# Kernel optimization log

Hardware: AMD Instinct MI355X
Metric: run time of the kernel (lower is better)

## Reference

```python
import jax, jax.numpy as jnp
import numpy as np
import math

B, L, D = 2, 2048, 1024
H, HD = 16, 64          # num heads, head dim
R = 256                 # kv lora rank = D // 4
E, K, F = 8, 2, 1024    # routed experts, top_k, intermediate size


def rmsnorm(x, w, eps=1e-6):
    ms = jnp.mean(x * x, axis=-1, keepdims=True)
    return w * (x * jax.lax.rsqrt(ms + eps))


def setup_inputs() -> dict:
    key = jax.random.key(0)
    ks = jax.random.split(key, 16)
    s = 0.02
    return {
        "x": jax.random.normal(ks[0], (B, L, D), jnp.float32),
        "ln1_w": jnp.ones((D,), jnp.float32),
        "q_w": jax.random.normal(ks[1], (D, H * HD), jnp.float32) * s,
        "kvd_w": jax.random.normal(ks[2], (D, R), jnp.float32) * s,
        "kvn_w": jnp.ones((R,), jnp.float32),
        "kvu_w": jax.random.normal(ks[3], (R, 2 * H * HD), jnp.float32) * s,
        "o_w": jax.random.normal(ks[4], (H * HD, D), jnp.float32) * s,
        "ln2_w": jnp.ones((D,), jnp.float32),
        "gate_w": jax.random.normal(ks[5], (D, E), jnp.float32) * s,
        "sh_w1": jax.random.normal(ks[6], (D, F), jnp.float32) * s,
        "sh_w2": jax.random.normal(ks[7], (F, D), jnp.float32) * s,
        "sh_w3": jax.random.normal(ks[8], (D, F), jnp.float32) * s,
        "re_w1": jax.random.normal(ks[9], (E, D, F), jnp.float32) * s,
        "re_w2": jax.random.normal(ks[10], (E, F, D), jnp.float32) * s,
        "re_w3": jax.random.normal(ks[11], (E, D, F), jnp.float32) * s,
    }


def reference(x, ln1_w, q_w, kvd_w, kvn_w, kvu_w, o_w, ln2_w, gate_w,
              sh_w1, sh_w2, sh_w3, re_w1, re_w2, re_w3):
    # ---- MLHA attention with pre-RMSNorm and latent-compressed KV ----
    xn = rmsnorm(x, ln1_w)
    q = (xn @ q_w).reshape(B, L, H, HD)
    latent = rmsnorm(xn @ kvd_w, kvn_w)                 # [B,L,R]
    kv = latent @ kvu_w                                 # [B,L,2*H*HD]
    k, v = jnp.split(kv, 2, axis=-1)
    k = k.reshape(B, L, H, HD)
    v = v.reshape(B, L, H, HD)
    scores = jnp.einsum('bxhd,byhd->bhxy', q, k) / math.sqrt(HD)
    causal = jnp.tril(jnp.ones((L, L), bool))
    scores = jnp.where(causal, scores, -jnp.inf)
    attn = jax.nn.softmax(scores, axis=-1)
    attn_out = jnp.einsum('bhxy,byhd->bxhd', attn, v).reshape(B, L, H * HD)
    h = x + attn_out @ o_w

    # ---- MoE (inference: no jitter, expert_bias = 0, no bias update) ----
    hn = rmsnorm(h, ln2_w)
    flat = hn.reshape(-1, D)                            # [T,D], T=B*L
    # shared expert (SwiGLU)
    shared = (jax.nn.silu(flat @ sh_w1) * (flat @ sh_w3)) @ sh_w2
    # router
    logits = flat @ gate_w                              # [T,E]
    probs = jax.nn.softmax(logits, axis=-1)
    topw, topi = jax.lax.top_k(probs, K)                # [T,K]
    topw = topw / jnp.sum(topw, axis=-1, keepdims=True)
    # per-token per-expert combine weight [T,E]
    combine = jnp.sum(topw[..., None] * jax.nn.one_hot(topi, E, dtype=flat.dtype), axis=1)
    # all routed experts densely, then masked combine (same math as masked loop)
    h1 = jnp.einsum('td,edf->etf', flat, re_w1)
    h3 = jnp.einsum('td,edf->etf', flat, re_w3)
    eo = jnp.einsum('etf,efd->etd', jax.nn.silu(h1) * h3, re_w2)
    routed = jnp.einsum('te,etd->td', combine, eo)
    moe_out = (shared + routed).reshape(B, L, D)
    return h + moe_out, probs
```

## Files before the change

### kernel.cpp

```cpp
#include <hip/hip_runtime.h>
#include <hip/hip_bf16.h>
#include <cstdint>
#include <cstddef>

typedef unsigned short u16;
typedef unsigned int u32;
typedef __attribute__((ext_vector_type(8))) short bf16x8;
typedef __attribute__((ext_vector_type(4))) float f32x4;

static constexpr int Bb = 2, Ll = 2048, Dd = 1024, Hh = 16, Rr = 256, Ee = 8, Ff = 1024;
static constexpr int Tt = Bb * Ll;
static constexpr float QSCALE = 0.18033688011112042f;

__device__ __forceinline__ u16 f2bf(float f){
  union { float f; u32 u; } v; v.f = f;
  u32 u = v.u;
  u32 r = u + 0x7FFFu + ((u >> 16) & 1u);
  return (u16)(r >> 16);
}
__device__ __forceinline__ float bf2f(u16 b){
  union { u32 u; float f; } v; v.u = ((u32)b) << 16; return v.f;
}

#define GLDS(gp, lp) __builtin_amdgcn_global_load_lds( \
    (const __attribute__((address_space(1))) unsigned int*)(gp), \
    (__attribute__((address_space(3))) unsigned int*)(lp), 16, 0, 0)

__global__ void transpose5(const float* __restrict__ q_w, const float* __restrict__ o_w,
                           const float* __restrict__ w1, const float* __restrict__ w3,
                           const float* __restrict__ w2,
                           u16* __restrict__ qkvdT, u16* __restrict__ oT,
                           u16* __restrict__ sh13T, u16* __restrict__ sh2T){
  const float* s; u16* d; int off, str;
  switch (blockIdx.z){
    case 0: s = q_w; d = qkvdT; off = 0; str = 1; break;
    case 1: s = o_w; d = oT;    off = 0; str = 1; break;
    case 2: s = w1;  d = sh13T; off = 0; str = 2; break;
    case 3: s = w3;  d = sh13T; off = 1; str = 2; break;
    default: s = w2; d = sh2T;  off = 0; str = 1; break;
  }
  __shared__ float tile[32][33];
  int bx = blockIdx.x * 32, by = blockIdx.y * 32;
  int tx = threadIdx.x, ty = threadIdx.y;
  #pragma unroll
  for (int i = ty; i < 32; i += 8) tile[i][tx] = s[(size_t)(by + i) * 1024 + bx + tx];
  __syncthreads();
  #pragma unroll
  for (int i = ty; i < 32; i += 8)
    d[(size_t)(off + (bx + i) * str) * 1024 + by + tx] = f2bf(tile[tx][i]);
}

__global__ void transposeEx(const float* __restrict__ re_w1, const float* __restrict__ re_w3,
                            const float* __restrict__ re_w2,
                            u16* __restrict__ re13T, u16* __restrict__ re2T){
  int z = blockIdx.z, which = z >> 3, e = z & 7;
  const float* s; u16* d; int off, str;
  size_t eo = (size_t)e * 1024 * 1024;
  if (which == 0){ s = re_w1 + eo; d = re13T + (size_t)e * 2048 * 1024; off = 0; str = 2; }
  else if (which == 1){ s = re_w3 + eo; d = re13T + (size_t)e * 2048 * 1024; off = 1; str = 2; }
  else { s = re_w2 + eo; d = re2T + (size_t)e * 1024 * 1024; off = 0; str = 1; }
  __shared__ float tile[32][33];
  int bx = blockIdx.x * 32, by = blockIdx.y * 32;
  int tx = threadIdx.x, ty = threadIdx.y;
  #pragma unroll
  for (int i = ty; i < 32; i += 8) tile[i][tx] = s[(size_t)(by + i) * 1024 + bx + tx];
  __syncthreads();
  #pragma unroll
  for (int i = ty; i < 32; i += 8)
    d[(size_t)(off + (bx + i) * str) * 1024 + by + tx] = f2bf(tile[tx][i]);
}

__global__ void transpose_conv(const float* __restrict__ src, u16* __restrict__ dst,
                               int K, int N, int dstOff){
  __shared__ float tile[32][33];
  int bx = blockIdx.x * 32, by = blockIdx.y * 32;
  int tx = threadIdx.x, ty = threadIdx.y;
  #pragma unroll
  for (int i = ty; i < 32; i += 8) tile[i][tx] = src[(size_t)(by + i) * N + bx + tx];
  __syncthreads();
  #pragma unroll
  for (int i = ty; i < 32; i += 8)
    dst[(size_t)(dstOff + bx + i) * K + by + tx] = f2bf(tile[tx][i]);
}

template<int DIM>
__global__ void rmsnorm_kernel(const float* __restrict__ x, const float* __restrict__ w,
                               u16* __restrict__ out){
  int t = blockIdx.x;
  const float* xr = x + (size_t)t * DIM;
  u16* orow = out + (size_t)t * DIM;
  int tid = threadIdx.x;
  constexpr int NT = 256;
  constexpr int PER = DIM / NT > 0 ? DIM / NT : 1;
  float vals[PER];
  float ss = 0.f;
  #pragma unroll
  for (int i = 0; i < PER; i++){
    int d = tid + i * NT;
    float v = (d < DIM) ? xr[d] : 0.f;
    vals[i] = v; ss += v * v;
  }
  __shared__ float red[4];
  for (int m = 32; m; m >>= 1) ss += __shfl_xor(ss, m, 64);
  if ((tid & 63) == 0) red[tid >> 6] = ss;
  __syncthreads();
  float tot = red[0] + red[1] + red[2] + red[3];
  float rn = rsqrtf(tot / DIM + 1e-6f);
  #pragma unroll
  for (int i = 0; i < PER; i++){
    int d = tid + i * NT;
    if (d < DIM) orow[d] = f2bf(vals[i] * rn * w[d]);
  }
}

__global__ void router_kernel(const float* __restrict__ h, const float* __restrict__ ln2w,
                              const float* __restrict__ gate,
                              float* __restrict__ probs_out,
                              int* __restrict__ topi, float* __restrict__ topw,
                              u16* __restrict__ hn){
  int t = blockIdx.x; int tid = threadIdx.x;
  const float* hr = h + (size_t)t * Dd;
  float v[4]; float ss = 0.f;
  #pragma unroll
  for (int i = 0; i < 4; i++){ float x = hr[tid + i * 256]; v[i] = x; ss += x * x; }
  __shared__ float red[4];
  for (int m = 32; m; m >>= 1) ss += __shfl_xor(ss, m, 64);
  if ((tid & 63) == 0) red[tid >> 6] = ss;
  __syncthreads();
  float rn = rsqrtf((red[0] + red[1] + red[2] + red[3]) / Dd + 1e-6f);
  float p[8];
  #pragma unroll
  for (int e = 0; e < 8; e++) p[e] = 0.f;
  #pragma unroll
  for (int i = 0; i < 4; i++){
    int d = tid + i * 256;
    float hv = v[i] * rn * ln2w[d];
    hn[(size_t)t * Dd + d] = f2bf(hv);
    const float* g = gate + (size_t)d * 8;
    #pragma unroll
    for (int e = 0; e < 8; e++) p[e] += hv * g[e];
  }
  #pragma unroll
  for (int e = 0; e < 8; e++){
    float x = p[e];
    for (int m = 32; m; m >>= 1) x += __shfl_xor(x, m, 64);
    p[e] = x;
  }
  __shared__ float pe[4][8];
  if ((tid & 63) == 0){ for (int e = 0; e < 8; e++) pe[tid >> 6][e] = p[e]; }
  __syncthreads();
  if (tid == 0){
    float lg[8];
    for (int e = 0; e < 8; e++) lg[e] = pe[0][e] + pe[1][e] + pe[2][e] + pe[3][e];
    float mx = lg[0];
    for (int e = 1; e < 8; e++) mx = fmaxf(mx, lg[e]);
    float pr[8]; float s = 0.f;
    for (int e = 0; e < 8; e++){ pr[e] = __expf(lg[e] - mx); s += pr[e]; }
    float inv = 1.f / s;
    for (int e = 0; e < 8; e++) probs_out[(size_t)t * 8 + e] = pr[e] * inv;
    int i0 = 0;
    for (int e = 1; e < 8; e++) if (pr[e] > pr[i0]) i0 = e;
    int i1 = -1;
    for (int e = 0; e < 8; e++){ if (e == i0) continue; if (i1 < 0 || pr[e] > pr[i1]) i1 = e; }
    float w0 = pr[i0], w1 = pr[i1]; float wn = 1.f / (w0 + w1);
    topi[t * 2] = i0; topi[t * 2 + 1] = i1;
    topw[t * 2] = w0 * wn; topw[t * 2 + 1] = w1 * wn;
  }
}

__global__ void hist_kernel(const int* __restrict__ topi, int* __restrict__ counts){
  __shared__ int h[8];
  int tid = threadIdx.x;
  if (tid < 8) h[tid] = 0;
  __syncthreads();
  int base = blockIdx.x * 512;
  for (int i = tid; i < 512; i += 256) atomicAdd(&h[topi[base + i]], 1);
  __syncthreads();
  if (tid < 8) atomicAdd(&counts[tid], h[tid]);
}

__global__ void bucket_kernel(const int* __restrict__ topi, const float* __restrict__ topw,
                              const int* __restrict__ counts, int* __restrict__ cur,
                              int* __restrict__ entries, float* __restrict__ ew){
  __shared__ int lh[8], lbase[8], lcur[8], loffs[8];
  int tid = threadIdx.x;
  if (tid < 8) lh[tid] = 0;
  __syncthreads();
  int t = blockIdx.x * 256 + tid;
  int e0 = topi[t * 2], e1 = topi[t * 2 + 1];
  atomicAdd(&lh[e0], 1); atomicAdd(&lh[e1], 1);
  __syncthreads();
  if (tid == 0){
    int c = 0;
    for (int e = 0; e < 8; e++){ loffs[e] = c; c += counts[e]; }
  }
  if (tid < 8){ lbase[tid] = atomicAdd(&cur[tid], lh[tid]); lcur[tid] = 0; }
  __syncthreads();
  int p0 = atomicAdd(&lcur[e0], 1);
  int pos0 = loffs[e0] + lbase[e0] + p0;
  entries[pos0] = t; ew[pos0] = topw[t * 2];
  int p1 = atomicAdd(&lcur[e1], 1);
  int pos1 = loffs[e1] + lbase[e1] + p1;
  entries[pos1] = t; ew[pos1] = topw[t * 2 + 1];
}

template<int TM, int ROWMODE, int MODE>
__launch_bounds__(256)
__global__ void gemm_bt(const u16* __restrict__ A, const u16* __restrict__ Bt,
                        void* __restrict__ C, const float* __restrict__ res,
                        int M, int N, int K, int lda, int ldc,
                        const int* __restrict__ entries, const float* __restrict__ ew,
                        const int* __restrict__ counts,
                        float* __restrict__ outAt){
  constexpr int MTC = TM / 32;
  __shared__ __align__(16) u16 As[TM * 32];
  __shared__ __align__(16) u16 Bs[128 * 32];
  __shared__ int els[TM];
  __shared__ float ewl[TM];

  int e = (ROWMODE ? blockIdx.z : 0);
  const u16* Bte = Bt + (size_t)e * N * K;
  int cnt, off;
  if (ROWMODE == 0){ cnt = M; off = 0; }
  else {
    cnt = counts[e];
    off = 0;
    for (int i = 0; i < e; i++) off += counts[i];
  }
  int rt = blockIdx.y * TM;
  if (rt >= cnt) return;
  int cb = blockIdx.x * 128;
  int tid = threadIdx.x;

  if (ROWMODE >= 1){
    if (tid < TM){
      int r = rt + tid;
      els[tid] = (r < cnt) ? entries[off + r] : 0;
      ewl[tid] = (MODE == 4 && r < cnt) ? ew[off + r] : 0.f;
    }
    __syncthreads();
  }

  int sr = tid >> 2;
  int skc = (tid & 3) * 8;
  int rr0 = rt + sr, rr1 = rt + sr + 64;
  size_t ar0 = 0, ar1 = 0;
  if (ROWMODE == 0){ ar0 = (size_t)rr0; ar1 = (size_t)rr1; }
  else if (ROWMODE == 1){ ar0 = (size_t)els[sr];
                          ar1 = (TM == 128) ? (size_t)els[sr + 64] : 0; }
  else {
    int c0 = rr0 < cnt ? rr0 : (cnt - 1);
    int c1 = rr1 < cnt ? rr1 : (cnt - 1);
    ar0 = (size_t)off + c0; ar1 = (size_t)off + c1;
  }
  const u16* pa0 = A + ar0 * lda + skc;
  const u16* pa1 = A + ar1 * lda + skc;
  const u16* pb0 = Bte + (size_t)(cb + sr) * K + skc;
  const u16* pb1 = Bte + (size_t)(cb + sr + 64) * K + skc;
  u16* lA0 = &As[tid * 8];
  u16* lA1 = &As[(TM == 128 ? 2048 : 0) + tid * 8];
  u16* lB0 = &Bs[tid * 8];
  u16* lB1 = &Bs[2048 + tid * 8];

  int w = tid >> 6, lane = tid & 63;
  int wm = w >> 1, wn = w & 1;
  int quad = lane >> 4, l16 = lane & 15;

  f32x4 acc[MTC][4];
  const f32x4 zf = {0.f, 0.f, 0.f, 0.f};
  #pragma unroll
  for (int i = 0; i < MTC; i++)
    #pragma unroll
    for (int j = 0; j < 4; j++) acc[i][j] = zf;

  for (int k0 = 0; k0 < K; k0 += 32){
    __syncthreads();
    GLDS(pa0 + k0, lA0);
    if (TM == 128) GLDS(pa1 + k0, lA1);
    GLDS(pb0 + k0, lB0);
    GLDS(pb1 + k0, lB1);
    __syncthreads();
    bf16x8 af[MTC], bfr[4];
    #pragma unroll
    for (int mt = 0; mt < MTC; mt++)
      af[mt] = *(const bf16x8*)&As[(wm * (TM / 2) + mt * 16 + l16) * 32 + quad * 8];
    #pragma unroll
    for (int nt = 0; nt < 4; nt++)
      bfr[nt] = *(const bf16x8*)&Bs[(wn * 64 + nt * 16 + l16) * 32 + quad * 8];
    #pragma unroll
    for (int mt = 0; mt < MTC; mt++)
      #pragma unroll
      for (int nt = 0; nt < 4; nt++)
        acc[mt][nt] = __builtin_amdgcn_mfma_f32_16x16x32_bf16(af[mt], bfr[nt], acc[mt][nt], 0, 0, 0);
  }

  #pragma unroll
  for (int mt = 0; mt < MTC; mt++){
    #pragma unroll
    for (int nt = 0; nt < 4; nt++){
      #pragma unroll
      for (int r = 0; r < 4; r++){
        int row = wm * (TM / 2) + mt * 16 + quad * 4 + r;
        int col = cb + wn * 64 + nt * 16 + l16;
        int rr = rt + row;
        float v = acc[mt][nt][r];
        if (MODE == 6){
          float pv = __shfl_xor(v, 1, 64);
          if (rr < cnt && (l16 & 1) == 0){
            float sl = v / (1.f + __expf(-v));
            size_t crow = (size_t)((ROWMODE == 1) ? (off + rr) : rr);
            ((u16*)C)[crow * ldc + (col >> 1)] = f2bf(sl * pv);
          }
          continue;
        }
        if (rr >= cnt) continue;
        if (MODE == 0){
          size_t ci = (size_t)((ROWMODE == 1) ? (off + rr) : rr) * ldc + col;
          ((u16*)C)[ci] = f2bf(v);
        } else if (MODE == 1){
          size_t ci = (size_t)rr * ldc + col;
          ((float*)C)[ci] = v + res[ci];
        } else if (MODE == 5){
          if (col < 1024) ((u16*)C)[(size_t)rr * 1024 + col] = f2bf(v * QSCALE);
          else            outAt[(size_t)rr * 256 + (col - 1024)] = v;
        } else {
          int tok = els[row];
          atomicAdd(&outAt[(size_t)tok * ldc + col], ewl[row] * v);
        }
      }
    }
  }
}

#define RBAR() __builtin_amdgcn_s_barrier()
#define VMCNT8() do{ asm volatile("s_waitcnt vmcnt(8)" ::: "memory"); \
                     __builtin_amdgcn_sched_barrier(0); }while(0)
#define VMCNT0() do{ asm volatile("s_waitcnt vmcnt(0)" ::: "memory"); \
                     __builtin_amdgcn_sched_barrier(0); }while(0)
#define MMQ(MQ, NQ, FA, FB) do{ \
  _Pragma("unroll") \
  for (int m4_ = 0; m4_ < 4; m4_++){ \
    _Pragma("unroll") \
    for (int n2_ = 0; n2_ < 2; n2_++){ \
      acc[(MQ)*4+m4_][(NQ)*2+n2_] = __builtin_amdgcn_mfma_f32_16x16x32_bf16(FA[m4_][0], FB[n2_][0], acc[(MQ)*4+m4_][(NQ)*2+n2_], 0, 0, 0); \
      acc[(MQ)*4+m4_][(NQ)*2+n2_] = __builtin_amdgcn_mfma_f32_16x16x32_bf16(FA[m4_][1], FB[n2_][1], acc[(MQ)*4+m4_][(NQ)*2+n2_], 0, 0, 0); \
    } \
  } }while(0)
#define RDA(DST, BB, MQ) do{ \
  _Pragma("unroll") \
  for (int m4_ = 0; m4_ < 4; m4_++){ \
    const char* p_ = (const char*)(&As[BB][0]) + (size_t)(wm*128 + (MQ)*64 + m4_*16 + l16)*128; \
    DST[m4_][0] = *(const bf16x8*)(p_ + offk0); \
    DST[m4_][1] = *(const bf16x8*)(p_ + offk1); \
  } }while(0)
#define RDB(DST, BB, NQ) do{ \
  _Pragma("unroll") \
  for (int n2_ = 0; n2_ < 2; n2_++){ \
    const char* p_ = (const char*)(&Bs[BB][0]) + (size_t)(wn*64 + (NQ)*32 + n2_*16 + l16)*128; \
    DST[n2_][0] = *(const bf16x8*)(p_ + offk0); \
    DST[n2_][1] = *(const bf16x8*)(p_ + offk1); \
  } }while(0)
#define STGA(SB, H, KT) do{ \
  GLDS(gA[(H)*2+0] + (size_t)(KT)*64, &As[SB][((H)*128 +  0)*64] + (size_t)tid*8); \
  GLDS(gA[(H)*2+1] + (size_t)(KT)*64, &As[SB][((H)*128 + 64)*64] + (size_t)tid*8); }while(0)
#define STGB(SB, H, KT) do{ \
  GLDS(gB[(H)*2+0] + (size_t)(KT)*64, &Bs[SB][((H)*128 +  0)*64] + (size_t)tid*8); \
  GLDS(gB[(H)*2+1] + (size_t)(KT)*64, &Bs[SB][((H)*128 + 64)*64] + (size_t)tid*8); }while(0)

__launch_bounds__(512, 2)
__global__ void gemm256_up(const u16* __restrict__ A,
                           const u16* __restrict__ sh13, const u16* __restrict__ re13,
                           u16* __restrict__ shg, u16* __restrict__ gr,
                           const int* __restrict__ entries, const int* __restrict__ counts){
  __shared__ __align__(16) u16 As[2][256 * 64];
  __shared__ __align__(16) u16 Bs[2][256 * 64];

  int e = blockIdx.z;
  int cnt, off = 0;
  if (e < 8){
    cnt = counts[e];
    for (int i = 0; i < e; i++) off += counts[i];
  } else cnt = Tt;
  int rt = blockIdx.y * 256;
  if (rt >= cnt) return;
  int cb = blockIdx.x * 256;
  const u16* Bte = (e < 8) ? (re13 + (size_t)e * 2048 * 1024) : sh13;
  u16* Cb = (e < 8) ? gr : shg;

  int tid = threadIdx.x;
  int w = tid >> 6, lane = tid & 63, quad = lane >> 4, l16 = lane & 15;
  int wm = w >> 2, wn = w & 3;
  int swz = (l16 & 7) << 4;
  int offk0 = (quad * 16) ^ swz;
  int offk1 = (64 + quad * 16) ^ swz;

  int trow = tid >> 3;
  int sk = ((((tid & 7) << 4) ^ ((trow & 7) << 4)) >> 1);
  const u16* gA[4]; const u16* gB[4];
  #pragma unroll
  for (int i = 0; i < 4; i++){
    int r = i * 64 + trow;
    int garow;
    if (e < 8){
      int idx = rt + r; if (idx >= cnt) idx = cnt - 1;
      garow = entries[off + idx];
    } else garow = rt + r;
    gA[i] = A + (size_t)garow * 1024 + sk;
    gB[i] = Bte + (size_t)(cb + r) * 1024 + sk;
  }

  f32x4 acc[8][4];
  const f32x4 zf = {0.f, 0.f, 0.f, 0.f};
  #pragma unroll
  for (int i = 0; i < 8; i++)
    #pragma unroll
    for (int j = 0; j < 4; j++) acc[i][j] = zf;

  auto tile = [&](int b, int t2, bool stg){
    bf16x8 fa0[4][2], fa1[4][2], fb0[2][2], fb1[2][2];
    RDA(fa0, b, 0); RDB(fb0, b, 0);
    RBAR();
    __builtin_amdgcn_s_setprio(1); MMQ(0, 0, fa0, fb0); __builtin_amdgcn_s_setprio(0);
    RBAR();
    RDB(fb1, b, 1);
    RBAR();
    __builtin_amdgcn_s_setprio(1); MMQ(0, 1, fa0, fb1); __builtin_amdgcn_s_setprio(0);
    RBAR();
    RDA(fa1, b, 1);
    RBAR();
    __builtin_amdgcn_s_setprio(1); MMQ(1, 0, fa1, fb0); __builtin_amdgcn_s_setprio(0);
    RBAR();
    if (stg){ STGB(b, 0, t2); STGB(b, 1, t2); STGA(b, 0, t2); STGA(b, 1, t2); }
    __builtin_amdgcn_s_setprio(1); MMQ(1, 1, fa1, fb1); __builtin_amdgcn_s_setprio(0);
  };

  STGB(0, 0, 0); STGB(0, 1, 0); STGA(0, 0, 0); STGA(0, 1, 0);
  STGB(1, 0, 1); STGB(1, 1, 1); STGA(1, 0, 1); STGA(1, 1, 1);
  VMCNT8();
  RBAR();

  for (int t = 0; t < 14; ++t){
    tile(t & 1, t + 2, true);
    VMCNT8();
    RBAR();
  }
  tile(0, 0, false);
  VMCNT0();
  RBAR();
  tile(1, 0, false);

  #pragma unroll
  for (int mi = 0; mi < 8; mi++){
    #pragma unroll
    for (int ni = 0; ni < 4; ni++){
      #pragma unroll
      for (int r = 0; r < 4; r++){
        int row = wm * 128 + (mi >> 2) * 64 + (mi & 3) * 16 + quad * 4 + r;
        int col = cb + wn * 64 + (ni >> 1) * 32 + (ni & 1) * 16 + l16;
        float v = acc[mi][ni][r];
        float pv = __shfl_xor(v, 1, 64);
        int grow = rt + row;
        if (grow < cnt && (l16 & 1) == 0){
          float sl = v / (1.f + __expf(-v));
          size_t crow = (e < 8) ? (size_t)(off + grow) : (size_t)grow;
          Cb[crow * 1024 + (col >> 1)] = f2bf(sl * pv);
        }
      }
    }
  }
}

__global__ void vt_kernel(const u16* __restrict__ kv, u16* __restrict__ vt){
  __shared__ __align__(16) u16 t[64 * 72];
  int kt = blockIdx.x * 64, h = blockIdx.y, b = blockIdx.z;
  size_t bL = (size_t)b * Ll;
  int tid = threadIdx.x;
  int r = tid >> 2, c0 = (tid & 3) * 16;
  const u16* src = kv + (bL + kt + r) * 2048 + 1024 + h * 64 + c0;
  *(uint4*)&t[r * 72 + c0]     = *(const uint4*)(src);
  *(uint4*)&t[r * 72 + c0 + 8] = *(const uint4*)(src + 8);
  __syncthreads();
  int d = tid >> 2; int k0 = (tid & 3) * 16;
  u16 tmp[16];
  #pragma unroll
  for (int j = 0; j < 16; j++) tmp[j] = t[(k0 + j) * 72 + d];
  u16* dst = vt + ((size_t)(b * Hh + h) * 64 + d) * (size_t)Ll + kt + k0;
  *(uint4*)dst       = *(const uint4*)&tmp[0];
  *(uint4*)(dst + 8) = *(const uint4*)&tmp[8];
}

__launch_bounds__(256)
__global__ void attn_kernel(const u16* __restrict__ q, const u16* __restrict__ kv,
                            const u16* __restrict__ vt, u16* __restrict__ out){
  constexpr int LD = 72;
  __shared__ __align__(16) u16 Ks[2][64 * LD];
  __shared__ __align__(16) u16 Vs[2][64 * LD];
  __shared__ __align__(16) u16 Ps[64 * LD];
  int h = blockIdx.y, b = blockIdx.z;
  size_t bL = (size_t)b * Ll;
  int tid = threadIdx.x, w = tid >> 6, lane = tid & 63, quad = lane >> 4, l16 = lane & 15;
  int sr = tid >> 2, sc = (tid & 3) * 16;
  const u16* kbase = kv + (bL + sr) * 2048 + h * 64 + sc;
  const u16* vbase = vt + ((size_t)(b * Hh + h) * 64 + sr) * (size_t)Ll + sc;
  const f32x4 zf = {0.f, 0.f, 0.f, 0.f};

  #pragma unroll
  for (int pass = 0; pass < 2; pass++){
    int q0 = (pass ? (31 - (int)blockIdx.x) : (int)blockIdx.x) * 64;
    int qrow = q0 + w * 16 + l16;

    bf16x8 qf[2];
    #pragma unroll
    for (int ks = 0; ks < 2; ks++)
      qf[ks] = *(const bf16x8*)(q + (bL + qrow) * 1024 + h * 64 + ks * 32 + quad * 8);

    f32x4 oacc[4];
    #pragma unroll
    for (int dt = 0; dt < 4; dt++) oacc[dt] = zf;
    float mprev = -1e30f, lsum = 0.f;

    uint4 kr0 = *(const uint4*)(kbase);
    uint4 kr1 = *(const uint4*)(kbase + 8);
    uint4 vr0 = *(const uint4*)(vbase);
    uint4 vr1 = *(const uint4*)(vbase + 8);
    *(uint4*)&Ks[0][sr * LD + sc]     = kr0;
    *(uint4*)&Ks[0][sr * LD + sc + 8] = kr1;
    *(uint4*)&Vs[0][sr * LD + sc]     = vr0;
    *(uint4*)&Vs[0][sr * LD + sc + 8] = vr1;
    int cur = 0;
    __syncthreads();

    for (int kt = 0; kt <= q0; kt += 64){
      bool pfetch = (kt + 64 <= q0);
      if (pfetch){
        const u16* kp = kbase + (size_t)(kt + 64) * 2048;
        kr0 = *(const uint4*)(kp);
        kr1 = *(const uint4*)(kp + 8);
        const u16* vp = vbase + kt + 64;
        vr0 = *(const uint4*)(vp);
        vr1 = *(const uint4*)(vp + 8);
      }
      const u16* ksp = Ks[cur];
      const u16* vsp = Vs[cur];

      f32x4 sacc[4];
      #pragma unroll
      for (int mt = 0; mt < 4; mt++) sacc[mt] = zf;
      __builtin_amdgcn_s_setprio(1);
      #pragma unroll
      for (int ks = 0; ks < 2; ks++){
        #pragma unroll
        for (int mt = 0; mt < 4; mt++){
          bf16x8 kf = *(const bf16x8*)&ksp[(mt * 16 + l16) * LD + ks * 32 + quad * 8];
          sacc[mt] = __builtin_amdgcn_mfma_f32_16x16x32_bf16(kf, qf[ks], sacc[mt], 0, 0, 0);
        }
      }
      __builtin_amdgcn_s_setprio(0);

      bool diag = (kt == q0);
      int lq = w * 16 + l16;
      float sv[16]; float mx = -1e30f;
      #pragma unroll
      for (int mt = 0; mt < 4; mt++){
        #pragma unroll
        for (int r = 0; r < 4; r++){
          float s = sacc[mt][r];
          if (diag && (mt * 16 + quad * 4 + r > lq)) s = -1e30f;
          sv[mt * 4 + r] = s;
          mx = fmaxf(mx, s);
        }
      }
      mx = fmaxf(mx, __shfl_xor(mx, 16, 64));
      mx = fmaxf(mx, __shfl_xor(mx, 32, 64));
      if (!__all(mx <= mprev)){
        float mnew = fmaxf(mprev, mx);
        float alpha = exp2f(mprev - mnew);
        mprev = mnew;
        lsum *= alpha;
        #pragma unroll
        for (int dt = 0; dt < 4; dt++) oacc[dt] *= alpha;
      }
      float rs = 0.f;
      #pragma unroll
      for (int mt = 0; mt < 4; mt++){
        float p0 = exp2f(sv[mt * 4 + 0] - mprev);
        float p1 = exp2f(sv[mt * 4 + 1] - mprev);
        float p2 = exp2f(sv[mt * 4 + 2] - mprev);
        float p3 = exp2f(sv[mt * 4 + 3] - mprev);
        rs += p0 + p1 + p2 + p3;
        union { uint2 u; __hip_bfloat162 h2[2]; } pk;
        pk.h2[0] = __float22bfloat162_rn(make_float2(p0, p1));
        pk.h2[1] = __float22bfloat162_rn(make_float2(p2, p3));
        *(uint2*)&Ps[(w * 16 + l16) * LD + mt * 16 + quad * 4] = pk.u;
      }
      rs += __shfl_xor(rs, 16, 64);
      rs += __shfl_xor(rs, 32, 64);
      lsum += rs;

      __builtin_amdgcn_s_setprio(1);
      #pragma unroll
      for (int ks = 0; ks < 2; ks++){
        bf16x8 pfr = *(const bf16x8*)&Ps[(w * 16 + l16) * LD + ks * 32 + quad * 8];
        #pragma unroll
        for (int dt = 0; dt < 4; dt++){
          bf16x8 vf = *(const bf16x8*)&vsp[(dt * 16 + l16) * LD + ks * 32 + quad * 8];
          oacc[dt] = __builtin_amdgcn_mfma_f32_16x16x32_bf16(vf, pfr, oacc[dt], 0, 0, 0);
        }
      }
      __builtin_amdgcn_s_setprio(0);

      if (pfetch){
        int nb = cur ^ 1;
        *(uint4*)&Ks[nb][sr * LD + sc]     = kr0;
        *(uint4*)&Ks[nb][sr * LD + sc + 8] = kr1;
        *(uint4*)&Vs[nb][sr * LD + sc]     = vr0;
        *(uint4*)&Vs[nb][sr * LD + sc + 8] = vr1;
        cur = nb;
      }
      __syncthreads();
    }

    float inv = 1.f / lsum;
    #pragma unroll
    for (int dt = 0; dt < 4; dt++){
      union { uint2 u; __hip_bfloat162 h2[2]; } ov;
      ov.h2[0] = __float22bfloat162_rn(make_float2(oacc[dt][0] * inv, oacc[dt][1] * inv));
      ov.h2[1] = __float22bfloat162_rn(make_float2(oacc[dt][2] * inv, oacc[dt][3] * inv));
      *(uint2*)(out + (bL + qrow) * 1024 + h * 64 + dt * 16 + quad * 4) = ov.u;
    }
  }
}

extern "C" void kernel_launch(void* const* d_in, const int* in_sizes, int n_in,
                              void* d_out, int out_size, void* d_ws, size_t ws_size,
                              hipStream_t stream){
  const float* x     = (const float*)d_in[0];
  const float* ln1_w = (const float*)d_in[1];
  const float* q_w   = (const float*)d_in[2];
  const float* kvd_w = (const float*)d_in[3];
  const float* kvn_w = (const float*)d_in[4];
  const float* kvu_w = (const float*)d_in[5];
  const float* o_w   = (const float*)d_in[6];
  const float* ln2_w = (const float*)d_in[7];
  const float* gate_w= (const float*)d_in[8];
  const float* sh_w1 = (const float*)d_in[9];
  const float* sh_w2 = (const float*)d_in[10];
  const float* sh_w3 = (const float*)d_in[11];
  const float* re_w1 = (const float*)d_in[12];
  const float* re_w2 = (const float*)d_in[13];
  const float* re_w3 = (const float*)d_in[14];
  float* out = (float*)d_out;

  char* wp = (char*)d_ws;
  auto alloc = [&](size_t bytes)->char*{
    char* p = wp; wp += (bytes + 255) & ~(size_t)255; return p;
  };
  u16* qkvdT = (u16*)alloc((size_t)1280 * 1024 * 2);
  u16* kvuT  = (u16*)alloc((size_t)2048 * 256 * 2);
  u16* oT    = (u16*)alloc((size_t)1024 * 1024 * 2);
  u16* sh13T = (u16*)alloc((size_t)2048 * 1024 * 2);
  u16* sh2T  = (u16*)alloc((size_t)1024 * 1024 * 2);
  u16* re13T = (u16*)alloc((size_t)8 * 2048 * 1024 * 2);
  u16* re2T  = (u16*)alloc((size_t)8 * 1024 * 1024 * 2);
  u16* xn    = (u16*)alloc((size_t)Tt * 1024 * 2);
  u16* qbuf  = (u16*)alloc((size_t)Tt * 1024 * 2);
  float* latpre = (float*)alloc((size_t)Tt * 256 * 4);
  u16* lat   = (u16*)alloc((size_t)Tt * 256 * 2);
  u16* kvbuf = (u16*)alloc((size_t)Tt * 2048 * 2);
  u16* attnb = (u16*)alloc((size_t)Tt * 1024 * 2);
  float* hbuf = (float*)alloc((size_t)Tt * 1024 * 4);
  u16* vtb   = (u16*)alloc((size_t)Bb * Hh * 64 * Ll * 2);
  u16* gr    = (u16*)alloc((size_t)Tt * 2 * 1024 * 2);
  int* counts = (int*)alloc(32);
  int* cur    = (int*)alloc(32);
  int* topi   = (int*)alloc((size_t)Tt * 2 * 4);
  float* topw = (float*)alloc((size_t)Tt * 2 * 4);
  int* entries= (int*)alloc((size_t)Tt * 2 * 4);
  float* ewt  = (float*)alloc((size_t)Tt * 2 * 4);
  (void)ws_size; (void)n_in; (void)in_sizes; (void)out_size;

  hipMemsetAsync(counts, 0, 32, stream);
  hipMemsetAsync(cur, 0, 32, stream);

  dim3 tb(32, 8);
  transpose5<<<dim3(32, 32, 5), tb, 0, stream>>>(q_w, o_w, sh_w1, sh_w3, sh_w2,
                                                 qkvdT, oT, sh13T, sh2T);
  transpose_conv<<<dim3(8, 32, 1), tb, 0, stream>>>(kvd_w, qkvdT, 1024, 256, 1024);
  transpose_conv<<<dim3(64, 8, 1), tb, 0, stream>>>(kvu_w, kvuT, 256, 2048, 0);
  transposeEx<<<dim3(32, 32, 24), tb, 0, stream>>>(re_w1, re_w3, re_w2, re13T, re2T);

  rmsnorm_kernel<1024><<<Tt, 256, 0, stream>>>(x, ln1_w, xn);

  gemm_bt<64,0,5><<<dim3(10, 64), 256, 0, stream>>>(xn, qkvdT, qbuf, nullptr,
      Tt, 1280, 1024, 1024, 1024, nullptr, nullptr, nullptr, latpre);
  rmsnorm_kernel<256><<<Tt, 256, 0, stream>>>(latpre, kvn_w, lat);
  gemm_bt<128,0,0><<<dim3(16, 32), 256, 0, stream>>>(lat, kvuT, kvbuf, nullptr,
      Tt, 2048, 256, 256, 2048, nullptr, nullptr, nullptr, nullptr);
  vt_kernel<<<dim3(32, 16, 2), 256, 0, stream>>>(kvbuf, vtb);
  attn_kernel<<<dim3(16, 16, 2), 256, 0, stream>>>(qbuf, kvbuf, vtb, attnb);
  gemm_bt<64,0,1><<<dim3(8, 64), 256, 0, stream>>>(attnb, oT, hbuf, x,
      Tt, 1024, 1024, 1024, 1024, nullptr, nullptr, nullptr, nullptr);
  router_kernel<<<Tt, 256, 0, stream>>>(hbuf, ln2_w, gate_w, out + (size_t)Tt * Dd,
                                        topi, topw, xn);
  hist_kernel<<<16, 256, 0, stream>>>(topi, counts);
  bucket_kernel<<<16, 256, 0, stream>>>(topi, topw, counts, cur, entries, ewt);

  gemm256_up<<<dim3(8, 16, 9), 512, 0, stream>>>(xn, sh13T, re13T, kvbuf, gr,
                                                 entries, counts);

  gemm_bt<64,0,1><<<dim3(8, 64), 256, 0, stream>>>(kvbuf, sh2T, out, hbuf,
      Tt, 1024, 1024, 1024, 1024, nullptr, nullptr, nullptr, nullptr);
  gemm_bt<128,2,4><<<dim3(8, 32, 8), 256, 0, stream>>>(gr, re2T, nullptr, nullptr,
      Tt, 1024, 1024, 1024, 1024, entries, ewt, counts, out);
}
```

Before: 551.1 us.

## Restructure MoE GEMM tile loop: load all fragments, then batch MFMAs

The per-tile schedule in the expert up-projection GEMM now reads all A/B fragments from LDS up front, then issues all four MFMA quadrants back-to-back under high priority. It drops the interleaved barriers between quadrants and issues the global-to-LDS staging for the next tile after the compute instead of before the last quadrant. Fewer barriers should reduce synchronization stalls, at the cost of more live fragment registers and less overlap between LDS reads and MFMAs.

Measured after the change: 547.1 us. Within noise of the previous version (-0.7%).

```diff
diff --git a/kernel.cpp b/kernel.cpp
--- a/kernel.cpp
+++ b/kernel.cpp
@@ -333,6 +333,7 @@
 }
 
 #define RBAR() __builtin_amdgcn_s_barrier()
+#define SBAR0() __builtin_amdgcn_sched_barrier(0)
 #define VMCNT8() do{ asm volatile("s_waitcnt vmcnt(8)" ::: "memory"); \
                      __builtin_amdgcn_sched_barrier(0); }while(0)
 #define VMCNT0() do{ asm volatile("s_waitcnt vmcnt(0)" ::: "memory"); \
@@ -416,22 +417,25 @@
     #pragma unroll
     for (int j = 0; j < 4; j++) acc[i][j] = zf;
 
-  auto tile = [&](int b, int t2, bool stg){
+  auto tile = [&](int b, int t2, int mode){
     bf16x8 fa0[4][2], fa1[4][2], fb0[2][2], fb1[2][2];
     RDA(fa0, b, 0); RDB(fb0, b, 0);
+    RDB(fb1, b, 1); RDA(fa1, b, 1);
+    __builtin_amdgcn_s_setprio(1);
+    MMQ(0, 0, fa0, fb0); MMQ(0, 1, fa0, fb1);
+    MMQ(1, 0, fa1, fb0); MMQ(1, 1, fa1, fb1);
+    __builtin_amdgcn_s_setprio(0);
+    if (mode == 2) return;
+    SBAR0();
     RBAR();
-    __builtin_amdgcn_s_setprio(1); MMQ(0, 0, fa0, fb0); __builtin_amdgcn_s_setprio(0);
+    if (mode == 0){
+      STGB(b, 0, t2); STGB(b, 1, t2); STGA(b, 0, t2); STGA(b, 1, t2);
+      VMCNT8();
+    } else {
+      VMCNT0();
+    }
     RBAR();
-    RDB(fb1, b, 1);
-    RBAR();
-    __builtin_amdgcn_s_setprio(1); MMQ(0, 1, fa0, fb1); __builtin_amdgcn_s_setprio(0);
-    RBAR();
-    RDA(fa1, b, 1);
-    RBAR();
-    __builtin_amdgcn_s_setprio(1); MMQ(1, 0, fa1, fb0); __builtin_amdgcn_s_setprio(0);
-    RBAR();
-    if (stg){ STGB(b, 0, t2); STGB(b, 1, t2); STGA(b, 0, t2); STGA(b, 1, t2); }
-    __builtin_amdgcn_s_setprio(1); MMQ(1, 1, fa1, fb1); __builtin_amdgcn_s_setprio(0);
+    SBAR0();
   };
 
   STGB(0, 0, 0); STGB(0, 1, 0); STGA(0, 0, 0); STGA(0, 1, 0);
@@ -439,15 +443,9 @@
   VMCNT8();
   RBAR();
 
-  for (int t = 0; t < 14; ++t){
-    tile(t & 1, t + 2, true);
-    VMCNT8();
-    RBAR();
-  }
-  tile(0, 0, false);
-  VMCNT0();
-  RBAR();
-  tile(1, 0, false);
+  for (int t = 0; t < 14; ++t) tile(t & 1, t + 2, 0);
+  tile(0, 0, 1);
+  tile(1, 0, 2);
 
   #pragma unroll
   for (int mi = 0; mi < 8; mi++){
```
